# Performance work log

Measured on AMD Instinct MI355X. Metric: run time of the kernel, lower is better.

## Reference

```python
import jax, jax.numpy as jnp
import numpy as np

N = 8192      # number of tree nodes
IN = 1024     # in_dim
M = 1024      # effective mem_dim = 2 * mem_dim_init
K = 8         # max children (complete 8-ary tree)


def _linear_init(key, out_dim, in_dim):
    k1, k2 = jax.random.split(key)
    s = 1.0 / np.sqrt(in_dim)
    w = jax.random.uniform(k1, (out_dim, in_dim), minval=-s, maxval=s, dtype=jnp.float32)
    b = jax.random.uniform(k2, (out_dim,), minval=-s, maxval=s, dtype=jnp.float32)
    return w, b


def setup_inputs() -> dict:
    key = jax.random.key(0)
    ks = jax.random.split(key, 5)
    w_ioux, b_ioux = _linear_init(ks[0], 3 * M, IN)
    w_iouh, b_iouh = _linear_init(ks[1], 3 * M, M)
    w_fx, b_fx = _linear_init(ks[2], M, IN)
    w_fh, b_fh = _linear_init(ks[3], M, M)
    inputs = jax.random.normal(ks[4], (N, IN), dtype=jnp.float32)
    # Complete K-ary tree: children of node p are p*K+1 .. p*K+K (clipped).
    # Pad with index N, which addresses an always-zero dummy row.
    ch = np.full((N, K), N, dtype=np.int32)
    for j in range(K):
        idx = np.arange(N) * K + 1 + j
        valid = idx < N
        ch[valid, j] = idx[valid]
    return dict(inputs=inputs, children=jnp.asarray(ch),
                w_ioux=w_ioux, b_ioux=b_ioux, w_iouh=w_iouh, b_iouh=b_iouh,
                w_fx=w_fx, b_fx=b_fx, w_fh=w_fh, b_fh=b_fh)


def reference(inputs, children, w_ioux, b_ioux, w_iouh, b_iouh, w_fx, b_fx, w_fh, b_fh):
    # Precompute the input-side projections for all nodes at once.
    iou_x = inputs @ w_ioux.T + b_ioux   # [N, 3M]
    fx_x = inputs @ w_fx.T + b_fx        # [N, M]
    h0 = jnp.zeros((N + 1, M), inputs.dtype)  # row N is the zero pad slot
    c0 = jnp.zeros((N + 1, M), inputs.dtype)

    def step(carry, t):
        h_buf, c_buf = carry
        ch = children[t]           # [K] child indices (pad = N -> zero rows)
        ch_h = h_buf[ch]           # [K, M] real child h's
        ch_c = c_buf[ch]           # [K, M] real child c's
        # Faithful to original: for internal nodes child_c/child_h are SWAPPED,
        # so the 'child_h_sum' and f-gate inputs use the real c's, while the
        # forgotten memory (fc) multiplies the real h's. Leaves: all zeros.
        csum = ch_c.sum(0)                                   # [M]
        iou = iou_x[t] + csum @ w_iouh.T + b_iouh            # [3M]
        i_g, o_g, u_g = jnp.split(iou, 3)
        i_g = jax.nn.sigmoid(i_g)
        o_g = jax.nn.sigmoid(o_g)
        u_g = jnp.tanh(u_g)
        f = jax.nn.sigmoid(ch_c @ w_fh.T + b_fh + fx_x[t])   # [K, M]
        c = i_g * u_g + (f * ch_h).sum(0)                    # [M]
        h = o_g * jnp.tanh(c)
        return (h_buf.at[t].set(h), c_buf.at[t].set(c)), None

    # Children always have larger indices than their parent, so processing
    # t = N-1 .. 0 matches the original reverse-BFS (leaves-first) order.
    order = jnp.arange(N - 1, -1, -1)
    (h_buf, c_buf), _ = jax.lax.scan(step, (h0, c0), order)
    root_h = h_buf[0][None, :]   # [1, M]
    root_c = c_buf[0][None, :]   # [1, M]
    return root_h, root_c
```

## Files before the change

kernel.cpp:

```cpp
#include <hip/hip_runtime.h>

typedef __bf16 bf16x8 __attribute__((ext_vector_type(8)));
typedef __attribute__((ext_vector_type(4))) float f4;

#define AS1 __attribute__((address_space(1)))
#define AS3 __attribute__((address_space(3)))

__device__ __forceinline__ unsigned short f2bf(float f) {
    union { float f; unsigned int u; } x; x.f = f;
    return (unsigned short)((x.u + 0x7fffu + ((x.u >> 16) & 1u)) >> 16);
}
__device__ __forceinline__ float bf2f(unsigned short u) {
    union { unsigned int u; float f; } x; x.u = (unsigned int)u << 16;
    return x.f;
}
__device__ __forceinline__ float fsigm(float x) {
    return __builtin_amdgcn_rcpf(1.f + __expf(-x));
}
__device__ __forceinline__ float ftanh(float x) {
    return 1.f - 2.f * __builtin_amdgcn_rcpf(1.f + __expf(2.f * x));
}
__device__ __forceinline__ void gload_lds16(const unsigned short* g, unsigned short* l) {
    __builtin_amdgcn_global_load_lds((const AS1 unsigned int*)g, (AS3 unsigned int*)l, 16, 0, 0);
}

__global__ void prep_all_k(const float* __restrict__ inputs, const float* __restrict__ w_ioux,
                           const float* __restrict__ w_fx, const float* __restrict__ w_iouh,
                           const float* __restrict__ w_fh,
                           const float* __restrict__ b_ioux, const float* __restrict__ b_iouh,
                           const float* __restrict__ b_fx, const float* __restrict__ b_fh,
                           unsigned short* __restrict__ Xbf, unsigned short* __restrict__ Wiouxbf,
                           unsigned short* __restrict__ Wfxbf, unsigned short* __restrict__ Whbf,
                           unsigned short* __restrict__ Wfhbf,
                           float* __restrict__ bias_iou, float* __restrict__ bias_f,
                           unsigned short* __restrict__ c_bf, unsigned short* __restrict__ h_bf) {
    int b = blockIdx.x;
    if (b < 16384) {
        int idx = b * 256 + threadIdx.x;
        const float* src; unsigned short* dst; int rel;
        if (idx < 2097152)      { src = inputs; dst = Xbf;     rel = idx; }
        else if (idx < 2883584) { src = w_ioux; dst = Wiouxbf; rel = idx - 2097152; }
        else if (idx < 3145728) { src = w_fx;   dst = Wfxbf;   rel = idx - 2883584; }
        else if (idx < 3932160) { src = w_iouh; dst = Whbf;    rel = idx - 3145728; }
        else                    { src = w_fh;   dst = Wfhbf;   rel = idx - 3932160; }
        float4 v = reinterpret_cast<const float4*>(src)[rel];
        ushort4 o; o.x = f2bf(v.x); o.y = f2bf(v.y); o.z = f2bf(v.z); o.w = f2bf(v.w);
        reinterpret_cast<ushort4*>(dst)[rel] = o;
    } else if (b < 16400) {
        int idx = (b - 16384) * 256 + threadIdx.x;
        if (idx < 3072) bias_iou[idx] = b_ioux[idx] + b_iouh[idx];
        else { int j = idx - 3072; bias_f[j] = b_fx[j] + b_fh[j]; }
    } else {
        int j = (b - 16400) * 256 + threadIdx.x;
        size_t o = (size_t)8192 * 1024 + j;
        c_bf[o] = 0; h_bf[o] = 0;
    }
}

__device__ __forceinline__ void gemm_core(const unsigned short* __restrict__ A,
                                          const unsigned short* __restrict__ B,
                                          int M, int K, int tile_m, int tile_n,
                                          unsigned short* lsA, unsigned short* lsB,
                                          f4 acc[4][4]) {
    const int tid = threadIdx.x;
    const int l = tid & 63, wid = tid >> 6;
    const int wm = wid >> 1, wn = wid & 1;
    const int fr = l & 15, q = l >> 4;

#pragma unroll
    for (int i = 0; i < 4; ++i)
#pragma unroll
        for (int j = 0; j < 4; ++j) acc[i][j] = (f4){0.f, 0.f, 0.f, 0.f};

    const int srow = tid >> 2;
    const int scol = (tid & 3) * 8;
    const unsigned short* pa0 = A + (size_t)min(tile_m + srow, M - 1) * K + scol;
    const unsigned short* pa1 = A + (size_t)min(tile_m + 64 + srow, M - 1) * K + scol;
    const unsigned short* pb0 = B + (size_t)(tile_n + srow) * K + scol;
    const unsigned short* pb1 = B + (size_t)(tile_n + 64 + srow) * K + scol;
    unsigned short* la0 = lsA + tid * 8;
    unsigned short* la1 = lsA + 2048 + tid * 8;
    unsigned short* lb0 = lsB + tid * 8;
    unsigned short* lb1 = lsB + 2048 + tid * 8;

    for (int k0 = 0; k0 < K; k0 += 32) {
        __syncthreads();
        gload_lds16(pa0 + k0, la0);
        gload_lds16(pa1 + k0, la1);
        gload_lds16(pb0 + k0, lb0);
        gload_lds16(pb1 + k0, lb1);
        __syncthreads();
        bf16x8 af[4], bq[4];
#pragma unroll
        for (int f = 0; f < 4; ++f)
            af[f] = *reinterpret_cast<const bf16x8*>(&lsA[(wm * 64 + f * 16 + fr) * 32 + q * 8]);
#pragma unroll
        for (int f = 0; f < 4; ++f)
            bq[f] = *reinterpret_cast<const bf16x8*>(&lsB[(wn * 64 + f * 16 + fr) * 32 + q * 8]);
#pragma unroll
        for (int i = 0; i < 4; ++i)
#pragma unroll
            for (int j = 0; j < 4; ++j)
                acc[i][j] = __builtin_amdgcn_mfma_f32_16x16x32_bf16(af[i], bq[j], acc[i][j], 0, 0, 0);
    }
}

__global__ __launch_bounds__(256)
void gemm_big_k(const unsigned short* __restrict__ Xbf, const unsigned short* __restrict__ Wioux,
                const unsigned short* __restrict__ Wfx,
                const float* __restrict__ bias_iou, const float* __restrict__ bias_f,
                unsigned short* __restrict__ P_iou, unsigned short* __restrict__ P_f) {
    __shared__ unsigned short lsA[4096];
    __shared__ unsigned short lsB[4096];
    int b = blockIdx.x;
    const unsigned short* Bp; unsigned short* Cp; const float* biasp;
    int ldc, tm, tn, M;
    if (b < 1536) {
        tm = (b & 63) * 128; tn = (b >> 6) * 128;
        Bp = Wioux; Cp = P_iou; biasp = bias_iou; ldc = 3072; M = 8192;
    } else {
        int bb = b - 1536;
        tm = (bb & 7) * 128; tn = (bb >> 3) * 128;
        Bp = Wfx; Cp = P_f; biasp = bias_f; ldc = 1024; M = 1024;
    }
    f4 acc[4][4];
    gemm_core(Xbf, Bp, M, 1024, tm, tn, lsA, lsB, acc);

    const int l = threadIdx.x & 63, wid = threadIdx.x >> 6;
    const int wm = wid >> 1, wn = wid & 1;
    const int fr = l & 15, q = l >> 4;
#pragma unroll
    for (int i = 0; i < 4; ++i)
#pragma unroll
        for (int j = 0; j < 4; ++j) {
            int col = tn + wn * 64 + fr + j * 16;
            float bv = biasp[col];
#pragma unroll
            for (int r = 0; r < 4; ++r) {
                int row = tm + wm * 64 + q * 4 + i * 16 + r;
                Cp[(size_t)row * ldc + col] = f2bf(acc[i][j][r] + bv);
            }
        }
}

__global__ void leaf_act_k(const unsigned short* __restrict__ P_iou,
                           unsigned short* __restrict__ h_bf, unsigned short* __restrict__ c_bf) {
    int idx = blockIdx.x * blockDim.x + threadIdx.x;
    int t = 1024 + (idx >> 8);
    int j = (idx & 255) * 4;
    const unsigned short* p = P_iou + (size_t)t * 3072 + j;
    ushort4 pi = *reinterpret_cast<const ushort4*>(p);
    ushort4 po = *reinterpret_cast<const ushort4*>(p + 1024);
    ushort4 pu = *reinterpret_cast<const ushort4*>(p + 2048);
    ushort4 cb, hb;
    float c0, c1, c2, c3;
    c0 = fsigm(bf2f(pi.x)) * ftanh(bf2f(pu.x)); hb.x = f2bf(fsigm(bf2f(po.x)) * ftanh(c0)); cb.x = f2bf(c0);
    c1 = fsigm(bf2f(pi.y)) * ftanh(bf2f(pu.y)); hb.y = f2bf(fsigm(bf2f(po.y)) * ftanh(c1)); cb.y = f2bf(c1);
    c2 = fsigm(bf2f(pi.z)) * ftanh(bf2f(pu.z)); hb.z = f2bf(fsigm(bf2f(po.z)) * ftanh(c2)); cb.z = f2bf(c2);
    c3 = fsigm(bf2f(pi.w)) * ftanh(bf2f(pu.w)); hb.w = f2bf(fsigm(bf2f(po.w)) * ftanh(c3)); cb.w = f2bf(c3);
    size_t o = (size_t)t * 1024 + j;
    *reinterpret_cast<ushort4*>(c_bf + o) = cb;
    *reinterpret_cast<ushort4*>(h_bf + o) = hb;
}

__device__ __forceinline__ void gemm_core_db(const unsigned short* __restrict__ A,
                                             const unsigned short* __restrict__ B,
                                             int M, int tile_m, int tile_n,
                                             unsigned short* lsA, unsigned short* lsB,
                                             f4 acc[4][4]) {
    const int K = 1024;
    const int tid = threadIdx.x;
    const int l = tid & 63, wid = tid >> 6;
    const int wm = wid >> 1, wn = wid & 1;
    const int fr = l & 15, q = l >> 4;

#pragma unroll
    for (int i = 0; i < 4; ++i)
#pragma unroll
        for (int j = 0; j < 4; ++j) acc[i][j] = (f4){0.f, 0.f, 0.f, 0.f};

    const unsigned short* ga[4]; const unsigned short* gb[4];
    unsigned short *la[4], *lb[4];
#pragma unroll
    for (int i = 0; i < 4; ++i) {
        int chunk = i * 256 + tid;
        int row = chunk >> 3, slot = chunk & 7;
        int scol = (slot ^ (row & 7)) * 8;
        ga[i] = A + (size_t)min(tile_m + row, M - 1) * K + scol;
        gb[i] = B + (size_t)(tile_n + row) * K + scol;
        la[i] = lsA + chunk * 8;
        lb[i] = lsB + chunk * 8;
    }
#pragma unroll
    for (int i = 0; i < 4; ++i) gload_lds16(ga[i], la[i]);
#pragma unroll
    for (int i = 0; i < 4; ++i) gload_lds16(gb[i], lb[i]);

    int roffA[4], roffB[4];
#pragma unroll
    for (int f = 0; f < 4; ++f) {
        roffA[f] = (wm * 64 + f * 16 + fr) * 64;
        roffB[f] = (wn * 64 + f * 16 + fr) * 64;
    }
    const int sw = fr & 7;
    int cur = 0;
    for (int t = 0; t < 16; ++t) {
        if (t < 15) {
            int k0 = (t + 1) * 64;
            int nb = (cur ^ 1) * 8192;
#pragma unroll
            for (int i = 0; i < 4; ++i) gload_lds16(ga[i] + k0, la[i] + nb);
#pragma unroll
            for (int i = 0; i < 4; ++i) gload_lds16(gb[i] + k0, lb[i] + nb);
            asm volatile("s_waitcnt vmcnt(8)" ::: "memory");
        } else {
            asm volatile("s_waitcnt vmcnt(0)" ::: "memory");
        }
        __builtin_amdgcn_s_barrier();
        const unsigned short* bA = lsA + cur * 8192;
        const unsigned short* bB = lsB + cur * 8192;
        bf16x8 af[4][2], bq[4][2];
#pragma unroll
        for (int f = 0; f < 4; ++f)
#pragma unroll
            for (int s = 0; s < 2; ++s) {
                int sl = ((s * 4 + q) ^ sw) * 8;
                af[f][s] = *reinterpret_cast<const bf16x8*>(&bA[roffA[f] + sl]);
                bq[f][s] = *reinterpret_cast<const bf16x8*>(&bB[roffB[f] + sl]);
            }
#pragma unroll
        for (int s = 0; s < 2; ++s)
#pragma unroll
            for (int i = 0; i < 4; ++i)
#pragma unroll
                for (int j = 0; j < 4; ++j)
                    acc[i][j] = __builtin_amdgcn_mfma_f32_16x16x32_bf16(af[i][s], bq[j][s], acc[i][j], 0, 0, 0);
        __builtin_amdgcn_s_barrier();
        cur ^= 1;
    }
}

struct GDesc {
    const unsigned short* A;
    const unsigned short* B;
    float* C;
    int M;
    int ldc;
    int tiles_n;
    int tiles_total;
};

__global__ __launch_bounds__(256)
void gemm_dual_k(GDesc d0, GDesc d1) {
    __shared__ unsigned short lsA[16384];
    __shared__ unsigned short lsB[16384];
    int b = blockIdx.x;
    GDesc d; int bb;
    if (b < d0.tiles_total) { d = d0; bb = b; }
    else { d = d1; bb = b - d0.tiles_total; }
    const int tile_m = (bb / d.tiles_n) * 128;
    const int tile_n = (bb % d.tiles_n) * 128;
    f4 acc[4][4];
    gemm_core_db(d.A, d.B, d.M, tile_m, tile_n, lsA, lsB, acc);

    const int l = threadIdx.x & 63, wid = threadIdx.x >> 6;
    const int wm = wid >> 1, wn = wid & 1;
    const int fr = l & 15, q = l >> 4;
#pragma unroll
    for (int i = 0; i < 4; ++i)
#pragma unroll
        for (int j = 0; j < 4; ++j) {
            int col = tile_n + wn * 64 + fr + j * 16;
#pragma unroll
            for (int r = 0; r < 4; ++r) {
                int row = tile_m + wm * 64 + q * 4 + i * 16 + r;
                if (row < d.M) d.C[(size_t)row * d.ldc + col] = acc[i][j][r];
            }
        }
}

__global__ void csum_k(const unsigned short* __restrict__ c_bf, unsigned short* __restrict__ csum_bf,
                       int lo, int n) {
    int idx = blockIdx.x * blockDim.x + threadIdx.x;
    if (idx >= n * 1024) return;
    int tt = idx >> 10, j = idx & 1023;
    size_t base = ((size_t)(lo + tt) * 8 + 1) * 1024 + j;
    float s = 0.f;
#pragma unroll
    for (int k = 0; k < 8; ++k) s += bf2f(c_bf[base + (size_t)k * 1024]);
    csum_bf[idx] = f2bf(s);
}

__global__ void node_update_k(const unsigned short* __restrict__ P_iou,
                              const unsigned short* __restrict__ P_f,
                              const float* __restrict__ out_iouh, const float* __restrict__ out_f,
                              unsigned short* __restrict__ h_bf, unsigned short* __restrict__ c_bf,
                              float* __restrict__ out, int lo, int n) {
    int idx = blockIdx.x * blockDim.x + threadIdx.x;
    if (idx >= n * 1024) return;
    int tt = idx >> 10, j = idx & 1023;
    int t = lo + tt;
    const unsigned short* p = P_iou + (size_t)t * 3072;
    const float* oi = out_iouh + (size_t)tt * 3072;
    float ig = fsigm(bf2f(p[j]) + oi[j]);
    float og = fsigm(bf2f(p[1024 + j]) + oi[1024 + j]);
    float ug = ftanh(bf2f(p[2048 + j]) + oi[2048 + j]);
    float pf = bf2f(P_f[(size_t)t * 1024 + j]);
    float a = ig * ug;
#pragma unroll
    for (int k = 0; k < 8; ++k) {
        float fg = fsigm(pf + out_f[(size_t)(tt * 8 + k) * 1024 + j]);
        a += fg * bf2f(h_bf[(size_t)(t * 8 + 1 + k) * 1024 + j]);
    }
    float hh = og * ftanh(a);
    size_t o = (size_t)t * 1024 + j;
    c_bf[o] = f2bf(a); h_bf[o] = f2bf(hh);
    if (t == 0) { out[j] = hh; out[1024 + j] = a; }
}

extern "C" void kernel_launch(void* const* d_in, const int* in_sizes, int n_in,
                              void* d_out, int out_size, void* d_ws, size_t ws_size,
                              hipStream_t stream) {
    const float* inputs = (const float*)d_in[0];
    const float* w_ioux = (const float*)d_in[2];
    const float* b_ioux = (const float*)d_in[3];
    const float* w_iouh = (const float*)d_in[4];
    const float* b_iouh = (const float*)d_in[5];
    const float* w_fx   = (const float*)d_in[6];
    const float* b_fx   = (const float*)d_in[7];
    const float* w_fh   = (const float*)d_in[8];
    const float* b_fh   = (const float*)d_in[9];
    float* out = (float*)d_out;

    char* ws = (char*)d_ws;
    size_t off = 0;
    auto alloc = [&](size_t bytes) -> void* {
        void* p = ws + off;
        off += (bytes + 255) & ~(size_t)255;
        return p;
    };
    unsigned short* Xbf     = (unsigned short*)alloc((size_t)8192 * 1024 * 2);
    unsigned short* Wiouxbf = (unsigned short*)alloc((size_t)3072 * 1024 * 2);
    unsigned short* Wfxbf   = (unsigned short*)alloc((size_t)1024 * 1024 * 2);
    unsigned short* Whbf    = (unsigned short*)alloc((size_t)3072 * 1024 * 2);
    unsigned short* Wfhbf   = (unsigned short*)alloc((size_t)1024 * 1024 * 2);
    float* bias_iou         = (float*)alloc((size_t)3072 * 4);
    float* bias_f           = (float*)alloc((size_t)1024 * 4);
    unsigned short* P_iou   = (unsigned short*)alloc((size_t)8192 * 3072 * 2);
    unsigned short* P_f     = (unsigned short*)alloc((size_t)1024 * 1024 * 2);
    unsigned short* c_bf    = (unsigned short*)alloc((size_t)8193 * 1024 * 2);
    unsigned short* h_bf    = (unsigned short*)alloc((size_t)8193 * 1024 * 2);
    unsigned short* csum_bf = (unsigned short*)alloc((size_t)512 * 1024 * 2);
    float* out_iouh         = (float*)alloc((size_t)512 * 3072 * 4);
    float* out_f            = (float*)alloc((size_t)4096 * 1024 * 4);

    prep_all_k<<<dim3(16404), dim3(256), 0, stream>>>(
        inputs, w_ioux, w_fx, w_iouh, w_fh, b_ioux, b_iouh, b_fx, b_fh,
        Xbf, Wiouxbf, Wfxbf, Whbf, Wfhbf, bias_iou, bias_f, c_bf, h_bf);

    gemm_big_k<<<dim3(1600), dim3(256), 0, stream>>>(Xbf, Wiouxbf, Wfxbf,
                                                     bias_iou, bias_f, P_iou, P_f);
    leaf_act_k<<<dim3(7168), dim3(256), 0, stream>>>(P_iou, h_bf, c_bf);

    const int LV_LO[5] = {585, 73, 9, 1, 0};
    const int LV_N[5]  = {439, 512, 64, 8, 1};
    for (int lv = 0; lv < 5; ++lv) {
        int lo = LV_LO[lv], n = LV_N[lv];
        int nel = n * 1024;
        csum_k<<<dim3((nel + 255) / 256), dim3(256), 0, stream>>>(c_bf, csum_bf, lo, n);
        GDesc d0, d1;
        d0.A = csum_bf; d0.B = Whbf; d0.C = out_iouh;
        d0.M = n; d0.ldc = 3072; d0.tiles_n = 24;
        d0.tiles_total = ((n + 127) / 128) * 24;
        d1.A = c_bf + (size_t)(lo * 8 + 1) * 1024; d1.B = Wfhbf; d1.C = out_f;
        d1.M = 8 * n; d1.ldc = 1024; d1.tiles_n = 8;
        d1.tiles_total = ((8 * n + 127) / 128) * 8;
        gemm_dual_k<<<dim3(d0.tiles_total + d1.tiles_total), dim3(256), 0, stream>>>(d0, d1);
        node_update_k<<<dim3((nel + 255) / 256), dim3(256), 0, stream>>>(
            P_iou, P_f, out_iouh, out_f, h_bf, c_bf, out, lo, n);
    }
    (void)in_sizes; (void)n_in; (void)out_size; (void)ws_size;
}
```

Measured before the change: 240.7 us.

## Fuse last three tree levels into one persistent kernel with grid barriers

Result: slower. 271.3 us (+12.7%).

```diff
diff --git a/kernel.cpp b/kernel.cpp
--- a/kernel.cpp
+++ b/kernel.cpp
@@ -33,7 +33,8 @@
                            unsigned short* __restrict__ Wfxbf, unsigned short* __restrict__ Whbf,
                            unsigned short* __restrict__ Wfhbf,
                            float* __restrict__ bias_iou, float* __restrict__ bias_f,
-                           unsigned short* __restrict__ c_bf, unsigned short* __restrict__ h_bf) {
+                           unsigned short* __restrict__ c_bf, unsigned short* __restrict__ h_bf,
+                           unsigned int* __restrict__ arrive) {
     int b = blockIdx.x;
     if (b < 16384) {
         int idx = b * 256 + threadIdx.x;
@@ -50,18 +51,21 @@
         int idx = (b - 16384) * 256 + threadIdx.x;
         if (idx < 3072) bias_iou[idx] = b_ioux[idx] + b_iouh[idx];
         else { int j = idx - 3072; bias_f[j] = b_fx[j] + b_fh[j]; }
-    } else {
+    } else if (b < 16404) {
         int j = (b - 16400) * 256 + threadIdx.x;
         size_t o = (size_t)8192 * 1024 + j;
         c_bf[o] = 0; h_bf[o] = 0;
-    }
-}
-
-__device__ __forceinline__ void gemm_core(const unsigned short* __restrict__ A,
-                                          const unsigned short* __restrict__ B,
-                                          int M, int K, int tile_m, int tile_n,
-                                          unsigned short* lsA, unsigned short* lsB,
-                                          f4 acc[4][4]) {
+    } else {
+        if (threadIdx.x < 64) arrive[threadIdx.x] = 0;
+    }
+}
+
+__device__ __forceinline__ void gemm_core_db(const unsigned short* __restrict__ A,
+                                             const unsigned short* __restrict__ B,
+                                             int M, int tile_m, int tile_n,
+                                             unsigned short* lsA, unsigned short* lsB,
+                                             f4 acc[4][4]) {
+    const int K = 1024;
     const int tid = threadIdx.x;
     const int l = tid & 63, wid = tid >> 6;
     const int wm = wid >> 1, wn = wid & 1;
@@ -72,36 +76,64 @@
 #pragma unroll
         for (int j = 0; j < 4; ++j) acc[i][j] = (f4){0.f, 0.f, 0.f, 0.f};
 
-    const int srow = tid >> 2;
-    const int scol = (tid & 3) * 8;
-    const unsigned short* pa0 = A + (size_t)min(tile_m + srow, M - 1) * K + scol;
-    const unsigned short* pa1 = A + (size_t)min(tile_m + 64 + srow, M - 1) * K + scol;
-    const unsigned short* pb0 = B + (size_t)(tile_n + srow) * K + scol;
-    const unsigned short* pb1 = B + (size_t)(tile_n + 64 + srow) * K + scol;
-    unsigned short* la0 = lsA + tid * 8;
-    unsigned short* la1 = lsA + 2048 + tid * 8;
-    unsigned short* lb0 = lsB + tid * 8;
-    unsigned short* lb1 = lsB + 2048 + tid * 8;
-
-    for (int k0 = 0; k0 < K; k0 += 32) {
-        __syncthreads();
-        gload_lds16(pa0 + k0, la0);
-        gload_lds16(pa1 + k0, la1);
-        gload_lds16(pb0 + k0, lb0);
-        gload_lds16(pb1 + k0, lb1);
-        __syncthreads();
-        bf16x8 af[4], bq[4];
+    const unsigned short* ga[4]; const unsigned short* gb[4];
+    unsigned short *la[4], *lb[4];
+#pragma unroll
+    for (int i = 0; i < 4; ++i) {
+        int chunk = i * 256 + tid;
+        int row = chunk >> 3, slot = chunk & 7;
+        int scol = (slot ^ (row & 7)) * 8;
+        ga[i] = A + (size_t)min(tile_m + row, M - 1) * K + scol;
+        gb[i] = B + (size_t)(tile_n + row) * K + scol;
+        la[i] = lsA + chunk * 8;
+        lb[i] = lsB + chunk * 8;
+    }
+#pragma unroll
+    for (int i = 0; i < 4; ++i) gload_lds16(ga[i], la[i]);
+#pragma unroll
+    for (int i = 0; i < 4; ++i) gload_lds16(gb[i], lb[i]);
+
+    int roffA[4], roffB[4];
+#pragma unroll
+    for (int f = 0; f < 4; ++f) {
+        roffA[f] = (wm * 64 + f * 16 + fr) * 64;
+        roffB[f] = (wn * 64 + f * 16 + fr) * 64;
+    }
+    const int sw = fr & 7;
+    int cur = 0;
+    for (int t = 0; t < 16; ++t) {
+        if (t < 15) {
+            int k0 = (t + 1) * 64;
+            int nb = (cur ^ 1) * 8192;
+#pragma unroll
+            for (int i = 0; i < 4; ++i) gload_lds16(ga[i] + k0, la[i] + nb);
+#pragma unroll
+            for (int i = 0; i < 4; ++i) gload_lds16(gb[i] + k0, lb[i] + nb);
+            asm volatile("s_waitcnt vmcnt(8)" ::: "memory");
+        } else {
+            asm volatile("s_waitcnt vmcnt(0)" ::: "memory");
+        }
+        __builtin_amdgcn_s_barrier();
+        const unsigned short* bA = lsA + cur * 8192;
+        const unsigned short* bB = lsB + cur * 8192;
+        bf16x8 af[4][2], bq[4][2];
 #pragma unroll
         for (int f = 0; f < 4; ++f)
-            af[f] = *reinterpret_cast<const bf16x8*>(&lsA[(wm * 64 + f * 16 + fr) * 32 + q * 8]);
-#pragma unroll
-        for (int f = 0; f < 4; ++f)
-            bq[f] = *reinterpret_cast<const bf16x8*>(&lsB[(wn * 64 + f * 16 + fr) * 32 + q * 8]);
-#pragma unroll
-        for (int i = 0; i < 4; ++i)
-#pragma unroll
-            for (int j = 0; j < 4; ++j)
-                acc[i][j] = __builtin_amdgcn_mfma_f32_16x16x32_bf16(af[i], bq[j], acc[i][j], 0, 0, 0);
+#pragma unroll
+            for (int s = 0; s < 2; ++s) {
+                int sl = ((s * 4 + q) ^ sw) * 8;
+                af[f][s] = *reinterpret_cast<const bf16x8*>(&bA[roffA[f] + sl]);
+                bq[f][s] = *reinterpret_cast<const bf16x8*>(&bB[roffB[f] + sl]);
+            }
+#pragma unroll
+        for (int s = 0; s < 2; ++s)
+#pragma unroll
+            for (int i = 0; i < 4; ++i)
+#pragma unroll
+                for (int j = 0; j < 4; ++j)
+                    acc[i][j] = __builtin_amdgcn_mfma_f32_16x16x32_bf16(af[i][s], bq[j][s], acc[i][j], 0, 0, 0);
+        __builtin_amdgcn_s_barrier();
+        cur ^= 1;
     }
 }
 
@@ -110,8 +142,8 @@
                 const unsigned short* __restrict__ Wfx,
                 const float* __restrict__ bias_iou, const float* __restrict__ bias_f,
                 unsigned short* __restrict__ P_iou, unsigned short* __restrict__ P_f) {
-    __shared__ unsigned short lsA[4096];
-    __shared__ unsigned short lsB[4096];
+    __shared__ unsigned short lsA[16384];
+    __shared__ unsigned short lsB[16384];
     int b = blockIdx.x;
     const unsigned short* Bp; unsigned short* Cp; const float* biasp;
     int ldc, tm, tn, M;
@@ -124,7 +156,7 @@
         Bp = Wfx; Cp = P_f; biasp = bias_f; ldc = 1024; M = 1024;
     }
     f4 acc[4][4];
-    gemm_core(Xbf, Bp, M, 1024, tm, tn, lsA, lsB, acc);
+    gemm_core_db(Xbf, Bp, M, tm, tn, lsA, lsB, acc);
 
     const int l = threadIdx.x & 63, wid = threadIdx.x >> 6;
     const int wm = wid >> 1, wn = wid & 1;
@@ -163,81 +195,85 @@
     *reinterpret_cast<ushort4*>(h_bf + o) = hb;
 }
 
-__device__ __forceinline__ void gemm_core_db(const unsigned short* __restrict__ A,
-                                             const unsigned short* __restrict__ B,
-                                             int M, int tile_m, int tile_n,
-                                             unsigned short* lsA, unsigned short* lsB,
-                                             f4 acc[4][4]) {
-    const int K = 1024;
-    const int tid = threadIdx.x;
-    const int l = tid & 63, wid = tid >> 6;
-    const int wm = wid >> 1, wn = wid & 1;
-    const int fr = l & 15, q = l >> 4;
-
-#pragma unroll
-    for (int i = 0; i < 4; ++i)
-#pragma unroll
-        for (int j = 0; j < 4; ++j) acc[i][j] = (f4){0.f, 0.f, 0.f, 0.f};
-
-    const unsigned short* ga[4]; const unsigned short* gb[4];
-    unsigned short *la[4], *lb[4];
-#pragma unroll
-    for (int i = 0; i < 4; ++i) {
-        int chunk = i * 256 + tid;
-        int row = chunk >> 3, slot = chunk & 7;
-        int scol = (slot ^ (row & 7)) * 8;
-        ga[i] = A + (size_t)min(tile_m + row, M - 1) * K + scol;
-        gb[i] = B + (size_t)(tile_n + row) * K + scol;
-        la[i] = lsA + chunk * 8;
-        lb[i] = lsB + chunk * 8;
-    }
-#pragma unroll
-    for (int i = 0; i < 4; ++i) gload_lds16(ga[i], la[i]);
-#pragma unroll
-    for (int i = 0; i < 4; ++i) gload_lds16(gb[i], lb[i]);
-
-    int roffA[4], roffB[4];
-#pragma unroll
-    for (int f = 0; f < 4; ++f) {
-        roffA[f] = (wm * 64 + f * 16 + fr) * 64;
-        roffB[f] = (wn * 64 + f * 16 + fr) * 64;
-    }
-    const int sw = fr & 7;
-    int cur = 0;
-    for (int t = 0; t < 16; ++t) {
-        if (t < 15) {
-            int k0 = (t + 1) * 64;
-            int nb = (cur ^ 1) * 8192;
-#pragma unroll
-            for (int i = 0; i < 4; ++i) gload_lds16(ga[i] + k0, la[i] + nb);
-#pragma unroll
-            for (int i = 0; i < 4; ++i) gload_lds16(gb[i] + k0, lb[i] + nb);
-            asm volatile("s_waitcnt vmcnt(8)" ::: "memory");
-        } else {
-            asm volatile("s_waitcnt vmcnt(0)" ::: "memory");
-        }
-        __builtin_amdgcn_s_barrier();
-        const unsigned short* bA = lsA + cur * 8192;
-        const unsigned short* bB = lsB + cur * 8192;
-        bf16x8 af[4][2], bq[4][2];
-#pragma unroll
-        for (int f = 0; f < 4; ++f)
-#pragma unroll
-            for (int s = 0; s < 2; ++s) {
-                int sl = ((s * 4 + q) ^ sw) * 8;
-                af[f][s] = *reinterpret_cast<const bf16x8*>(&bA[roffA[f] + sl]);
-                bq[f][s] = *reinterpret_cast<const bf16x8*>(&bB[roffB[f] + sl]);
-            }
-#pragma unroll
-        for (int s = 0; s < 2; ++s)
-#pragma unroll
-            for (int i = 0; i < 4; ++i)
-#pragma unroll
-                for (int j = 0; j < 4; ++j)
-                    acc[i][j] = __builtin_amdgcn_mfma_f32_16x16x32_bf16(af[i][s], bq[j][s], acc[i][j], 0, 0, 0);
-        __builtin_amdgcn_s_barrier();
-        cur ^= 1;
-    }
+__device__ __forceinline__ void csum_dev(const unsigned short* __restrict__ c_bf,
+                                         unsigned short* __restrict__ csum_bf, int lo, int w) {
+    int tt = w >> 8, j = (w & 255) * 4;
+    size_t base = (size_t)((lo + tt) * 8 + 1) * 1024 + j;
+    float s0 = 0.f, s1 = 0.f, s2 = 0.f, s3 = 0.f;
+#pragma unroll
+    for (int k = 0; k < 8; ++k) {
+        ushort4 v = *reinterpret_cast<const ushort4*>(c_bf + base + (size_t)k * 1024);
+        s0 += bf2f(v.x); s1 += bf2f(v.y); s2 += bf2f(v.z); s3 += bf2f(v.w);
+    }
+    ushort4 o; o.x = f2bf(s0); o.y = f2bf(s1); o.z = f2bf(s2); o.w = f2bf(s3);
+    *reinterpret_cast<ushort4*>(csum_bf + (size_t)tt * 1024 + j) = o;
+}
+
+__device__ __forceinline__ void node_update_dev(
+    const unsigned short* __restrict__ P_iou, const unsigned short* __restrict__ P_f,
+    const float* __restrict__ out_iouh, const float* __restrict__ out_f,
+    unsigned short* __restrict__ h_bf, unsigned short* __restrict__ c_bf,
+    float* __restrict__ out, int lo, int w) {
+    int tt = w >> 8, j = (w & 255) * 4;
+    int t = lo + tt;
+    const unsigned short* p = P_iou + (size_t)t * 3072 + j;
+    ushort4 pi4 = *reinterpret_cast<const ushort4*>(p);
+    ushort4 po4 = *reinterpret_cast<const ushort4*>(p + 1024);
+    ushort4 pu4 = *reinterpret_cast<const ushort4*>(p + 2048);
+    const float* oi = out_iouh + (size_t)tt * 3072 + j;
+    float4 oii = *reinterpret_cast<const float4*>(oi);
+    float4 oio = *reinterpret_cast<const float4*>(oi + 1024);
+    float4 oiu = *reinterpret_cast<const float4*>(oi + 2048);
+    ushort4 pf4 = *reinterpret_cast<const ushort4*>(P_f + (size_t)t * 1024 + j);
+    float pf[4] = {bf2f(pf4.x), bf2f(pf4.y), bf2f(pf4.z), bf2f(pf4.w)};
+    float a[4], og[4];
+    a[0] = fsigm(bf2f(pi4.x) + oii.x) * ftanh(bf2f(pu4.x) + oiu.x);
+    a[1] = fsigm(bf2f(pi4.y) + oii.y) * ftanh(bf2f(pu4.y) + oiu.y);
+    a[2] = fsigm(bf2f(pi4.z) + oii.z) * ftanh(bf2f(pu4.z) + oiu.z);
+    a[3] = fsigm(bf2f(pi4.w) + oii.w) * ftanh(bf2f(pu4.w) + oiu.w);
+    og[0] = fsigm(bf2f(po4.x) + oio.x);
+    og[1] = fsigm(bf2f(po4.y) + oio.y);
+    og[2] = fsigm(bf2f(po4.z) + oio.z);
+    og[3] = fsigm(bf2f(po4.w) + oio.w);
+#pragma unroll
+    for (int k = 0; k < 8; ++k) {
+        float4 fo = *reinterpret_cast<const float4*>(out_f + (size_t)(tt * 8 + k) * 1024 + j);
+        ushort4 hc = *reinterpret_cast<const ushort4*>(h_bf + (size_t)(t * 8 + 1 + k) * 1024 + j);
+        a[0] += fsigm(pf[0] + fo.x) * bf2f(hc.x);
+        a[1] += fsigm(pf[1] + fo.y) * bf2f(hc.y);
+        a[2] += fsigm(pf[2] + fo.z) * bf2f(hc.z);
+        a[3] += fsigm(pf[3] + fo.w) * bf2f(hc.w);
+    }
+    float h0 = og[0] * ftanh(a[0]);
+    float h1 = og[1] * ftanh(a[1]);
+    float h2 = og[2] * ftanh(a[2]);
+    float h3 = og[3] * ftanh(a[3]);
+    size_t o = (size_t)t * 1024 + j;
+    ushort4 cb; cb.x = f2bf(a[0]); cb.y = f2bf(a[1]); cb.z = f2bf(a[2]); cb.w = f2bf(a[3]);
+    ushort4 hb; hb.x = f2bf(h0); hb.y = f2bf(h1); hb.z = f2bf(h2); hb.w = f2bf(h3);
+    *reinterpret_cast<ushort4*>(c_bf + o) = cb;
+    *reinterpret_cast<ushort4*>(h_bf + o) = hb;
+    if (t == 0) {
+        float4 hv; hv.x = h0; hv.y = h1; hv.z = h2; hv.w = h3;
+        float4 cv; cv.x = a[0]; cv.y = a[1]; cv.z = a[2]; cv.w = a[3];
+        *reinterpret_cast<float4*>(out + j) = hv;
+        *reinterpret_cast<float4*>(out + 1024 + j) = cv;
+    }
+}
+
+__global__ void csum_k(const unsigned short* __restrict__ c_bf, unsigned short* __restrict__ csum_bf,
+                       int lo, int n) {
+    int w = blockIdx.x * blockDim.x + threadIdx.x;
+    if (w < n * 256) csum_dev(c_bf, csum_bf, lo, w);
+}
+
+__global__ void node_update_k(const unsigned short* __restrict__ P_iou,
+                              const unsigned short* __restrict__ P_f,
+                              const float* __restrict__ out_iouh, const float* __restrict__ out_f,
+                              unsigned short* __restrict__ h_bf, unsigned short* __restrict__ c_bf,
+                              float* __restrict__ out, int lo, int n) {
+    int w = blockIdx.x * blockDim.x + threadIdx.x;
+    if (w < n * 256) node_update_dev(P_iou, P_f, out_iouh, out_f, h_bf, c_bf, out, lo, w);
 }
 
 struct GDesc {
@@ -279,43 +315,72 @@
         }
 }
 
-__global__ void csum_k(const unsigned short* __restrict__ c_bf, unsigned short* __restrict__ csum_bf,
-                       int lo, int n) {
-    int idx = blockIdx.x * blockDim.x + threadIdx.x;
-    if (idx >= n * 1024) return;
-    int tt = idx >> 10, j = idx & 1023;
-    size_t base = ((size_t)(lo + tt) * 8 + 1) * 1024 + j;
-    float s = 0.f;
-#pragma unroll
-    for (int k = 0; k < 8; ++k) s += bf2f(c_bf[base + (size_t)k * 1024]);
-    csum_bf[idx] = f2bf(s);
-}
-
-__global__ void node_update_k(const unsigned short* __restrict__ P_iou,
-                              const unsigned short* __restrict__ P_f,
-                              const float* __restrict__ out_iouh, const float* __restrict__ out_f,
-                              unsigned short* __restrict__ h_bf, unsigned short* __restrict__ c_bf,
-                              float* __restrict__ out, int lo, int n) {
-    int idx = blockIdx.x * blockDim.x + threadIdx.x;
-    if (idx >= n * 1024) return;
-    int tt = idx >> 10, j = idx & 1023;
-    int t = lo + tt;
-    const unsigned short* p = P_iou + (size_t)t * 3072;
-    const float* oi = out_iouh + (size_t)tt * 3072;
-    float ig = fsigm(bf2f(p[j]) + oi[j]);
-    float og = fsigm(bf2f(p[1024 + j]) + oi[1024 + j]);
-    float ug = ftanh(bf2f(p[2048 + j]) + oi[2048 + j]);
-    float pf = bf2f(P_f[(size_t)t * 1024 + j]);
-    float a = ig * ug;
-#pragma unroll
-    for (int k = 0; k < 8; ++k) {
-        float fg = fsigm(pf + out_f[(size_t)(tt * 8 + k) * 1024 + j]);
-        a += fg * bf2f(h_bf[(size_t)(t * 8 + 1 + k) * 1024 + j]);
-    }
-    float hh = og * ftanh(a);
-    size_t o = (size_t)t * 1024 + j;
-    c_bf[o] = f2bf(a); h_bf[o] = f2bf(hh);
-    if (t == 0) { out[j] = hh; out[1024 + j] = a; }
+#define TAIL_BLOCKS 64
+
+__device__ __forceinline__ void gbar(unsigned int* arrive, int round) {
+    __syncthreads();
+    if (threadIdx.x == 0) {
+        __threadfence();
+        __hip_atomic_fetch_add(arrive, 1u, __ATOMIC_RELEASE, __HIP_MEMORY_SCOPE_AGENT);
+        unsigned int target = (unsigned int)(round * TAIL_BLOCKS);
+        while (__hip_atomic_load(arrive, __ATOMIC_ACQUIRE, __HIP_MEMORY_SCOPE_AGENT) < target)
+            __builtin_amdgcn_s_sleep(8);
+    }
+    __syncthreads();
+}
+
+__global__ __launch_bounds__(256)
+void tail_k(unsigned short* __restrict__ c_bf, unsigned short* __restrict__ h_bf,
+            unsigned short* __restrict__ csum_bf,
+            const unsigned short* __restrict__ Whbf, const unsigned short* __restrict__ Wfhbf,
+            const unsigned short* __restrict__ P_iou, const unsigned short* __restrict__ P_f,
+            float* __restrict__ out_iouh, float* __restrict__ out_f,
+            float* __restrict__ out, unsigned int* __restrict__ arrive) {
+    __shared__ unsigned short lsA[16384];
+    __shared__ unsigned short lsB[16384];
+    const int LO[3] = {9, 1, 0};
+    const int NN[3] = {64, 8, 1};
+    int round = 0;
+    for (int lv = 0; lv < 3; ++lv) {
+        const int lo = LO[lv], n = NN[lv];
+        for (int w = blockIdx.x * 256 + threadIdx.x; w < n * 256; w += TAIL_BLOCKS * 256)
+            csum_dev(c_bf, csum_bf, lo, w);
+        gbar(arrive, ++round);
+        const int t1 = ((8 * n + 127) / 128) * 8;
+        for (int tile = blockIdx.x; tile < 24 + t1; tile += TAIL_BLOCKS) {
+            const unsigned short* A; const unsigned short* Bw; float* C;
+            int M, ldc, tm, tn;
+            if (tile < 24) {
+                A = csum_bf; Bw = Whbf; C = out_iouh; M = n; ldc = 3072;
+                tm = 0; tn = tile * 128;
+            } else {
+                int bb = tile - 24;
+                A = c_bf + (size_t)(lo * 8 + 1) * 1024; Bw = Wfhbf; C = out_f;
+                M = 8 * n; ldc = 1024;
+                tm = (bb >> 3) * 128; tn = (bb & 7) * 128;
+            }
+            f4 acc[4][4];
+            gemm_core_db(A, Bw, M, tm, tn, lsA, lsB, acc);
+            const int l = threadIdx.x & 63, wid = threadIdx.x >> 6;
+            const int wm = wid >> 1, wn = wid & 1;
+            const int fr = l & 15, q = l >> 4;
+#pragma unroll
+            for (int i = 0; i < 4; ++i)
+#pragma unroll
+                for (int j = 0; j < 4; ++j) {
+                    int col = tn + wn * 64 + fr + j * 16;
+#pragma unroll
+                    for (int r = 0; r < 4; ++r) {
+                        int row = tm + wm * 64 + q * 4 + i * 16 + r;
+                        if (row < M) C[(size_t)row * ldc + col] = acc[i][j][r];
+                    }
+                }
+        }
+        gbar(arrive, ++round);
+        for (int w = blockIdx.x * 256 + threadIdx.x; w < n * 256; w += TAIL_BLOCKS * 256)
+            node_update_dev(P_iou, P_f, out_iouh, out_f, h_bf, c_bf, out, lo, w);
+        gbar(arrive, ++round);
+    }
 }
 
 extern "C" void kernel_launch(void* const* d_in, const int* in_sizes, int n_in,
@@ -353,21 +418,21 @@
     unsigned short* csum_bf = (unsigned short*)alloc((size_t)512 * 1024 * 2);
     float* out_iouh         = (float*)alloc((size_t)512 * 3072 * 4);
     float* out_f            = (float*)alloc((size_t)4096 * 1024 * 4);
-
-    prep_all_k<<<dim3(16404), dim3(256), 0, stream>>>(
+    unsigned int* arrive    = (unsigned int*)alloc(256);
+
+    prep_all_k<<<dim3(16405), dim3(256), 0, stream>>>(
         inputs, w_ioux, w_fx, w_iouh, w_fh, b_ioux, b_iouh, b_fx, b_fh,
-        Xbf, Wiouxbf, Wfxbf, Whbf, Wfhbf, bias_iou, bias_f, c_bf, h_bf);
+        Xbf, Wiouxbf, Wfxbf, Whbf, Wfhbf, bias_iou, bias_f, c_bf, h_bf, arrive);
 
     gemm_big_k<<<dim3(1600), dim3(256), 0, stream>>>(Xbf, Wiouxbf, Wfxbf,
                                                      bias_iou, bias_f, P_iou, P_f);
     leaf_act_k<<<dim3(7168), dim3(256), 0, stream>>>(P_iou, h_bf, c_bf);
 
-    const int LV_LO[5] = {585, 73, 9, 1, 0};
-    const int LV_N[5]  = {439, 512, 64, 8, 1};
-    for (int lv = 0; lv < 5; ++lv) {
+    const int LV_LO[2] = {585, 73};
+    const int LV_N[2]  = {439, 512};
+    for (int lv = 0; lv < 2; ++lv) {
         int lo = LV_LO[lv], n = LV_N[lv];
-        int nel = n * 1024;
-        csum_k<<<dim3((nel + 255) / 256), dim3(256), 0, stream>>>(c_bf, csum_bf, lo, n);
+        csum_k<<<dim3(n), dim3(256), 0, stream>>>(c_bf, csum_bf, lo, n);
         GDesc d0, d1;
         d0.A = csum_bf; d0.B = Whbf; d0.C = out_iouh;
         d0.M = n; d0.ldc = 3072; d0.tiles_n = 24;
@@ -376,8 +441,10 @@
         d1.M = 8 * n; d1.ldc = 1024; d1.tiles_n = 8;
         d1.tiles_total = ((8 * n + 127) / 128) * 8;
         gemm_dual_k<<<dim3(d0.tiles_total + d1.tiles_total), dim3(256), 0, stream>>>(d0, d1);
-        node_update_k<<<dim3((nel + 255) / 256), dim3(256), 0, stream>>>(
+        node_update_k<<<dim3(n), dim3(256), 0, stream>>>(
             P_iou, P_f, out_iouh, out_f, h_bf, c_bf, out, lo, n);
     }
+    tail_k<<<dim3(TAIL_BLOCKS), dim3(256), 0, stream>>>(
+        c_bf, h_bf, csum_bf, Whbf, Wfhbf, P_iou, P_f, out_iouh, out_f, out, arrive);
     (void)in_sizes; (void)n_in; (void)out_size; (void)ws_size;
 }
```
